# Kernel optimization log

Hardware: AMD Instinct MI355X
Metric: run time of the kernel (lower is better)

The kernel has to match this reference:

```python
import jax, jax.numpy as jnp
import numpy as np
import math

DEPTH = 2
RATIOS = (0.5, 0.5)
K_PROP = 2  # Gra_inc(2)


def _prop(x, ei, ew, K=K_PROP):
    # GCN-style sym-normalized diffusion with implicit self-loops; Gra_inc(K)
    N = x.shape[0]
    row, col = ei[0], ei[1]
    deg = jax.ops.segment_sum(ew, row, num_segments=N) + 1.0  # +1 self-loop
    dinv = jax.lax.rsqrt(deg)
    norm = dinv[row] * ew * dinv[col]          # [E]
    self_n = (dinv * dinv)[:, None]            # [N,1]
    h, out = x, x
    for _ in range(K):
        h = jax.ops.segment_sum(norm[:, None] * h[col], row, num_segments=N) + self_n * h
        out = out + h
    return out


def _conv(x, ei, ew, W):
    return _prop(x @ W, ei, ew)


def _pool(x, ei, ew, pw, ratio):
    # PyG TopKPooling: score = tanh(x.pw/||pw||), keep top ceil(ratio*N) nodes,
    # gate features by score, relabel surviving edges (dropped edges -> weight 0).
    N = x.shape[0]
    k = int(math.ceil(ratio * N))
    score = jnp.tanh(x @ pw / jnp.linalg.norm(pw))
    val, perm = jax.lax.top_k(score, k)
    x2 = x[perm] * val[:, None]
    nm = jnp.full((N,), -1, jnp.int32).at[perm].set(jnp.arange(k, dtype=jnp.int32))
    r, c = nm[ei[0]], nm[ei[1]]
    kept = (r >= 0) & (c >= 0)
    ei2 = jnp.stack([jnp.where(kept, r, 0), jnp.where(kept, c, 0)])
    ew2 = jnp.where(kept, ew, 0.0)
    return x2, ei2, ew2, perm


def setup_inputs() -> dict:
    key = jax.random.key(0)
    ks = jax.random.split(key, 10)
    N, E, C_in, C_hid, C_out = 50000, 800000, 128, 128, 64
    def w(k, i, o):
        return jax.random.normal(k, (i, o), jnp.float32) / np.sqrt(i)
    return {
        "x": jax.random.normal(ks[0], (N, C_in), jnp.float32),
        "edge_index": jax.random.randint(ks[1], (2, E), 0, N, dtype=jnp.int32),
        "Wd0": w(ks[2], C_in, C_hid),
        "Wd1": w(ks[3], C_hid, C_hid),
        "Wd2": w(ks[4], C_hid, C_hid),
        "pw0": jax.random.normal(ks[5], (C_hid,), jnp.float32) / np.sqrt(C_hid),
        "pw1": jax.random.normal(ks[6], (C_hid,), jnp.float32) / np.sqrt(C_hid),
        "Wu0": w(ks[7], C_hid, C_hid),
        "Wu1": w(ks[8], C_hid, C_hid),
        "Wu2": w(ks[9], 2 * C_hid, C_out),
    }


def reference(x, edge_index, Wd0, Wd1, Wd2, pw0, pw1, Wu0, Wu1, Wu2):
    ei = edge_index
    ew = jnp.ones((ei.shape[1],), x.dtype)
    x = jax.nn.relu(_conv(x, ei, ew, Wd0))
    org = x
    xs, eis, ews, perms = [x], [ei], [ew], []
    for i, (pw, Wd) in enumerate(zip((pw0, pw1), (Wd1, Wd2))):
        x, ei, ew, perm = _pool(x, ei, ew, pw, RATIOS[i])
        x = jax.nn.relu(_conv(x, ei, ew, Wd))
        if i < DEPTH - 1:
            xs.append(x); eis.append(ei); ews.append(ew)
        perms.append(perm)
    for i, Wu in enumerate((Wu0, Wu1)):
        j = DEPTH - 1 - i
        res, ei, ew, perm = xs[j], eis[j], ews[j], perms[j]
        up = jnp.zeros_like(res).at[perm].set(x)
        x = res + up  # sum_res skip fusion
        x = _conv(x, ei, ew, Wu)
        if i < DEPTH - 1:
            x = jax.nn.relu(x)
    x = jnp.concatenate([x, org], axis=1)
    return _conv(x, ei, ew, Wu2)
```

## Files before the change

### kernel.cpp

```cpp
#include <hip/hip_runtime.h>
#include <hip/hip_bf16.h>
#include <stdint.h>

#define DEV __device__ __forceinline__

static constexpr int C_HID = 128;

DEV float4 f4_fma(float a, float4 w, float4 acc) {
  acc.x = fmaf(a, w.x, acc.x); acc.y = fmaf(a, w.y, acc.y);
  acc.z = fmaf(a, w.z, acc.z); acc.w = fmaf(a, w.w, acc.w);
  return acc;
}

__global__ void scorekeys_kernel(const float* __restrict__ x, const float* __restrict__ pw,
                                 float* __restrict__ score, unsigned long long* __restrict__ keys,
                                 int N) {
  int row = blockIdx.x * 4 + (threadIdx.x >> 6);
  int lane = threadIdx.x & 63;
  if (row >= N) return;
  float p0 = pw[lane], p1 = pw[lane + 64];
  float pn = p0 * p0 + p1 * p1;
  const float* xr = x + (size_t)row * C_HID;
  float s = xr[lane] * p0 + xr[lane + 64] * p1;
#pragma unroll
  for (int o = 32; o > 0; o >>= 1) {
    s += __shfl_xor(s, o, 64);
    pn += __shfl_xor(pn, o, 64);
  }
  if (lane == 0) {
    float sc = tanhf(s / sqrtf(pn));
    score[row] = sc;
    unsigned u = __float_as_uint(sc);
    u ^= (u >> 31) ? 0xFFFFFFFFu : 0x80000000u;
    keys[row] = (((unsigned long long)(~u)) << 16) | (unsigned)row;
  }
}

__global__ void select_init_kernel(unsigned long long* prefix, int* rem, int k, int* hist3) {
  int i = blockIdx.x * 256 + threadIdx.x;
  if (i == 0) { *prefix = 0ull; *rem = k; }
  for (int j = i; j < 3 * 65536; j += gridDim.x * 256) hist3[j] = 0;
}

__global__ void select_hist_kernel(const unsigned long long* __restrict__ keys, int N,
                                   const unsigned long long* __restrict__ prefix,
                                   int shift, unsigned long long M, int* __restrict__ hist) {
  int i = blockIdx.x * 256 + threadIdx.x;
  if (i >= N) return;
  unsigned long long P = *prefix;
  unsigned long long key = keys[i];
  if (((key ^ P) & M) == 0)
    atomicAdd(&hist[(int)((key >> shift) & 0xFFFF)], 1);
}

__global__ void select_find_kernel(const int* __restrict__ hist,
                                   unsigned long long* __restrict__ prefix,
                                   int* __restrict__ rem, int shift, int* __restrict__ ctr) {
  int t = threadIdx.x;
  int base = t * 64;
  int s = 0;
#pragma unroll
  for (int j = 0; j < 64; ++j) s += hist[base + j];
  int lane = t & 63, w = t >> 6;
  int v = s;
  for (int o = 1; o < 64; o <<= 1) { int u = __shfl_up(v, o, 64); if (lane >= o) v += u; }
  __shared__ int ws[16];
  if (lane == 63) ws[w] = v;
  __syncthreads();
  if (t < 16) {
    int u = ws[t];
    for (int o = 1; o < 16; o <<= 1) { int uu = __shfl_up(u, o, 64); if (t >= o) u += uu; }
    ws[t] = u;
  }
  __syncthreads();
  int incl = v + (w > 0 ? ws[w - 1] : 0);
  int excl = incl - s;
  int R = *rem;
  if (excl < R && incl >= R) {
    int c = excl, b = base;
    for (int j = 0; j < 64; ++j) {
      int h = hist[base + j];
      if (c + h >= R) { b = base + j; break; }
      c += h;
    }
    *prefix |= ((unsigned long long)b) << shift;
    *rem = R - c;
    if (shift == 0) *ctr = 0;
  }
}

__global__ void select_enum_kernel(const unsigned long long* __restrict__ keys, int N,
                                   const unsigned long long* __restrict__ Tptr,
                                   int* __restrict__ ctr, int* __restrict__ perm,
                                   int* __restrict__ nm) {
  int i = blockIdx.x * 256 + threadIdx.x;
  if (i >= N) return;
  unsigned long long T = *Tptr;
  if (keys[i] <= T) { int r = atomicAdd(ctr, 1); perm[r] = i; nm[i] = r; }
  else nm[i] = -1;
}

__global__ void pool_gather_kernel(const float* __restrict__ xold, const float* __restrict__ score,
                                   const int* __restrict__ perm, float* __restrict__ xnew, int k) {
  int j = blockIdx.x * 2 + (threadIdx.x >> 7);
  int f = threadIdx.x & 127;
  if (j >= k) return;
  int src = perm[j];
  xnew[(size_t)j * C_HID + f] = xold[(size_t)src * C_HID + f] * score[src];
}

DEV bool map_edge(int a, int b, const int* m0, const int* m1, int& r, int& c) {
  r = a; c = b;
  if (m0) { r = m0[r]; c = m0[c]; if ((r | c) < 0) return false; }
  if (m1) { r = m1[r]; c = m1[c]; if ((r | c) < 0) return false; }
  return true;
}

__global__ void edge_count_kernel(const int* __restrict__ ei, int E, int* __restrict__ cnt) {
  int e = blockIdx.x * 256 + threadIdx.x;
  if (e >= E) return;
  atomicAdd(&cnt[ei[e]], 1);
}

__global__ void edge_fill_kernel(const int* __restrict__ ei, int E,
                                 const int* __restrict__ rowptr, int* __restrict__ fc,
                                 int* __restrict__ colv) {
  int e = blockIdx.x * 256 + threadIdx.x;
  if (e >= E) return;
  int r = ei[e], c = ei[E + e];
  int pos = rowptr[r] + atomicAdd(&fc[r], 1);
  colv[pos] = c;
}

#define CEPT 7
__global__ __launch_bounds__(1024) void edge_count_compact_kernel(
    const int* __restrict__ ei, int E, const int* m0, const int* m1,
    int* __restrict__ cnt, int2* __restrict__ pairs, int* __restrict__ pctr) {
  int tid = threadIdx.x;
  int gbase = blockIdx.x * (1024 * CEPT) + tid;
  int rs[CEPT], cs[CEPT];
  int myn = 0;
#pragma unroll
  for (int i = 0; i < CEPT; ++i) {
    int e = gbase + i * 1024;
    int r, c;
    bool keep = (e < E) && map_edge(ei[e], ei[E + e], m0, m1, r, c);
    rs[i] = keep ? r : -1;
    cs[i] = keep ? c : 0;
    if (keep) { atomicAdd(&cnt[r], 1); ++myn; }
  }
  int lane = tid & 63, w = tid >> 6;
  int v = myn;
  for (int o = 1; o < 64; o <<= 1) { int u = __shfl_up(v, o, 64); if (lane >= o) v += u; }
  __shared__ int ws[16];
  __shared__ int bbase;
  if (lane == 63) ws[w] = v;
  __syncthreads();
  if (tid < 16) {
    int u = ws[tid];
    for (int o = 1; o < 16; o <<= 1) { int uu = __shfl_up(u, o, 64); if (tid >= o) u += uu; }
    ws[tid] = u;
  }
  __syncthreads();
  int excl = v - myn + (w > 0 ? ws[w - 1] : 0);
  if (tid == 1023) bbase = atomicAdd(pctr, excl + myn);
  __syncthreads();
  int pos = bbase + excl;
#pragma unroll
  for (int i = 0; i < CEPT; ++i)
    if (rs[i] >= 0) pairs[pos++] = make_int2(rs[i], cs[i]);
}

__global__ void edge_fill_compact_kernel(const int2* __restrict__ pairs, const int* __restrict__ pctr,
                                         const int* __restrict__ rowptr, int* __restrict__ fc,
                                         int* __restrict__ colv) {
  int i = blockIdx.x * 256 + threadIdx.x;
  if (i >= *pctr) return;
  int2 pr = pairs[i];
  int pos = rowptr[pr.x] + atomicAdd(&fc[pr.x], 1);
  colv[pos] = pr.y;
}

__global__ void scan_partial_kernel(const int* __restrict__ cnt, int n, int* __restrict__ bsum) {
  int i = blockIdx.x * 256 + threadIdx.x;
  int v = (i < n) ? cnt[i] : 0;
#pragma unroll
  for (int o = 32; o > 0; o >>= 1) v += __shfl_down(v, o, 64);
  __shared__ int ws[4];
  if ((threadIdx.x & 63) == 0) ws[threadIdx.x >> 6] = v;
  __syncthreads();
  if (threadIdx.x == 0) bsum[blockIdx.x] = ws[0] + ws[1] + ws[2] + ws[3];
}

__global__ void scan_blocksums_kernel(int* __restrict__ bsum, int nb) {
  int t = threadIdx.x;
  int v = (t < nb) ? bsum[t] : 0;
  int lane = t & 63, w = t >> 6;
  for (int o = 1; o < 64; o <<= 1) { int u = __shfl_up(v, o, 64); if (lane >= o) v += u; }
  __shared__ int ws[16];
  if (lane == 63) ws[w] = v;
  __syncthreads();
  if (t < 16) {
    int u = ws[t];
    for (int o = 1; o < 16; o <<= 1) { int uu = __shfl_up(u, o, 64); if (t >= o) u += uu; }
    ws[t] = u;
  }
  __syncthreads();
  if (t < nb) bsum[t] = v + (w > 0 ? ws[w - 1] : 0);
}

__global__ void scan_scatter_kernel(const int* __restrict__ cnt, int n,
                                    const int* __restrict__ bsum,
                                    int* __restrict__ rowptr, float* __restrict__ dinv,
                                    int* __restrict__ fc) {
  int i = blockIdx.x * 256 + threadIdx.x;
  int v = (i < n) ? cnt[i] : 0;
  int lane = threadIdx.x & 63, w = threadIdx.x >> 6;
  int s = v;
  for (int o = 1; o < 64; o <<= 1) { int u = __shfl_up(s, o, 64); if (lane >= o) s += u; }
  __shared__ int ws[4];
  __shared__ int wo[4];
  if (lane == 63) ws[w] = s;
  __syncthreads();
  if (threadIdx.x == 0) { int c = 0; for (int j = 0; j < 4; ++j) { wo[j] = c; c += ws[j]; } }
  __syncthreads();
  int excl = s - v + wo[w] + (blockIdx.x > 0 ? bsum[blockIdx.x - 1] : 0);
  if (i < n) {
    rowptr[i] = excl;
    dinv[i] = rsqrtf((float)v + 1.0f);
    fc[i] = 0;
    if (i == n - 1) rowptr[n] = excl + v;
  }
}

template <int FIRST, int RELU>
__global__ void spmm_kernel(const int* __restrict__ rowptr, const int* __restrict__ colv,
                            const float* __restrict__ dinv,
                            const float* __restrict__ h_in, const float* __restrict__ x0,
                            float* __restrict__ out, int M, int C) {
  int lanes = C >> 2;
  int rpb = 256 / lanes;
  int r = blockIdx.x * rpb + (int)threadIdx.x / lanes;
  int lane = (int)threadIdx.x % lanes;
  if (r >= M) return;
  float d = dinv[r];
  const float4* hin4 = (const float4*)h_in;
  size_t base = (size_t)r * lanes + lane;
  float4 self = hin4[base];
  float sn = d * d;
  float4 v = make_float4(sn * self.x, sn * self.y, sn * self.z, sn * self.w);
  int e0 = rowptr[r], e1 = rowptr[r + 1];
  int e = e0;
  for (; e + 8 <= e1; e += 8) {
    int cc[8];
#pragma unroll
    for (int i = 0; i < 8; ++i) cc[i] = colv[e + i];
    float4 hh[8];
#pragma unroll
    for (int i = 0; i < 8; ++i) hh[i] = hin4[(size_t)cc[i] * lanes + lane];
    float ww[8];
#pragma unroll
    for (int i = 0; i < 8; ++i) ww[i] = d * dinv[cc[i]];
#pragma unroll
    for (int i = 0; i < 8; ++i) v = f4_fma(ww[i], hh[i], v);
  }
  for (; e + 4 <= e1; e += 4) {
    int c0 = colv[e], c1 = colv[e + 1], c2 = colv[e + 2], c3 = colv[e + 3];
    float4 h0 = hin4[(size_t)c0 * lanes + lane];
    float4 h1 = hin4[(size_t)c1 * lanes + lane];
    float4 h2 = hin4[(size_t)c2 * lanes + lane];
    float4 h3 = hin4[(size_t)c3 * lanes + lane];
    float w0 = d * dinv[c0], w1 = d * dinv[c1], w2 = d * dinv[c2], w3 = d * dinv[c3];
    v = f4_fma(w0, h0, v); v = f4_fma(w1, h1, v);
    v = f4_fma(w2, h2, v); v = f4_fma(w3, h3, v);
  }
  for (; e < e1; ++e) {
    int c = colv[e];
    float w = d * dinv[c];
    float4 h = hin4[(size_t)c * lanes + lane];
    v = f4_fma(w, h, v);
  }
  if (FIRST) {
    ((float4*)out)[base] = v;
  } else {
    float4 a = ((const float4*)x0)[base];
    a.x += self.x + v.x; a.y += self.y + v.y; a.z += self.z + v.z; a.w += self.w + v.w;
    if (RELU) { a.x = fmaxf(a.x, 0.f); a.y = fmaxf(a.y, 0.f); a.z = fmaxf(a.z, 0.f); a.w = fmaxf(a.w, 0.f); }
    ((float4*)out)[base] = a;
  }
}

template <int NC, int KT, int SKIP, int ADDIN>
__global__ __launch_bounds__(256) void gemm_kernel(const float* __restrict__ A1, int K1,
                                                   const float* __restrict__ W,
                                                   float* __restrict__ Cd, int M,
                                                   const float* __restrict__ up,
                                                   const int* __restrict__ nm,
                                                   const float* __restrict__ addv) {
  constexpr int KTILE = 32;
  constexpr int AP = KTILE + 4;
  constexpr int CG = NC / 4;
  constexpr int RG = 256 / CG;
  constexpr int RPT = 64 / RG;
  __shared__ float Wl[KTILE * NC];
  __shared__ float Al[64 * AP];
  int tid = threadIdx.x;
  int r0 = blockIdx.x * 64;
  int cg = tid % CG, rg = tid / CG;
  float4 acc[RPT];
#pragma unroll
  for (int m = 0; m < RPT; ++m) acc[m] = make_float4(0.f, 0.f, 0.f, 0.f);

  for (int k0 = 0; k0 < KT; k0 += KTILE) {
    const float4* Wg = (const float4*)(W + (size_t)k0 * NC);
    for (int idx = tid; idx < KTILE * NC / 4; idx += 256)
      ((float4*)Wl)[idx] = Wg[idx];
#pragma unroll
    for (int s = 0; s < (64 * KTILE / 4) / 256; ++s) {
      int f4i = tid + s * 256;
      int row = f4i >> 3;
      int kk = (f4i & 7) << 2;
      int gr = r0 + row, gk = k0 + kk;
      float4 v = make_float4(0.f, 0.f, 0.f, 0.f);
      if (gr < M) {
        v = *(const float4*)(A1 + (size_t)gr * K1 + gk);
        if (SKIP) {
          int j = nm[gr];
          if (j >= 0) {
            float4 u = *(const float4*)(up + (size_t)j * K1 + gk);
            v.x += u.x; v.y += u.y; v.z += u.z; v.w += u.w;
          }
        }
      }
      *(float4*)&Al[row * AP + kk] = v;
    }
    __syncthreads();
#pragma unroll
    for (int kk0 = 0; kk0 < KTILE; kk0 += 4) {
      float4 a4[RPT];
#pragma unroll
      for (int m = 0; m < RPT; ++m)
        a4[m] = *(const float4*)&Al[(rg * RPT + m) * AP + kk0];
#pragma unroll
      for (int j = 0; j < 4; ++j) {
        float4 w = *(const float4*)&Wl[(kk0 + j) * NC + cg * 4];
#pragma unroll
        for (int m = 0; m < RPT; ++m) {
          float a = (j == 0) ? a4[m].x : (j == 1) ? a4[m].y : (j == 2) ? a4[m].z : a4[m].w;
          acc[m] = f4_fma(a, w, acc[m]);
        }
      }
    }
    __syncthreads();
  }
#pragma unroll
  for (int m = 0; m < RPT; ++m) {
    int gr = r0 + rg * RPT + m;
    if (gr < M) {
      float4 o = acc[m];
      if (ADDIN) {
        float4 u = *(const float4*)(addv + (size_t)gr * NC + cg * 4);
        o.x += u.x; o.y += u.y; o.z += u.z; o.w += u.w;
      }
      *(float4*)(Cd + (size_t)gr * NC + cg * 4) = o;
    }
  }
}

extern "C" void kernel_launch(void* const* d_in, const int* in_sizes, int n_in,
                              void* d_out, int out_size, void* d_ws, size_t ws_size,
                              hipStream_t stream) {
  const float* x   = (const float*)d_in[0];
  const int*   ei  = (const int*)d_in[1];
  const float* Wd0 = (const float*)d_in[2];
  const float* Wd1 = (const float*)d_in[3];
  const float* Wd2 = (const float*)d_in[4];
  const float* pw0 = (const float*)d_in[5];
  const float* pw1 = (const float*)d_in[6];
  const float* Wu0 = (const float*)d_in[7];
  const float* Wu1 = (const float*)d_in[8];
  const float* Wu2 = (const float*)d_in[9];
  float* out = (float*)d_out;

  const int C = C_HID;
  int N0 = in_sizes[0] / C;
  int E  = in_sizes[1] / 2;
  int k1 = (N0 + 1) / 2;
  int k2 = (k1 + 1) / 2;

  char* p = (char*)d_ws;
  auto alloc = [&](size_t bytes) { char* q = p; p += (bytes + 255) & ~(size_t)255; return q; };
  float* org   = (float*)alloc((size_t)N0 * C * 4);
  float* b0    = (float*)alloc((size_t)N0 * C * 4);
  float* b1    = (float*)alloc((size_t)N0 * C * 4);
  float* b2    = (float*)alloc((size_t)N0 * C * 4);
  float* x1res = (float*)alloc((size_t)k1 * C * 4);
  float* score = (float*)alloc((size_t)N0 * 4);
  unsigned long long* keys = (unsigned long long*)alloc((size_t)N0 * 8);
  int* perm0 = (int*)alloc((size_t)k1 * 4);
  int* perm1 = (int*)alloc((size_t)k2 * 4);
  int* map0  = (int*)alloc((size_t)N0 * 4);
  int* map1  = (int*)alloc((size_t)k1 * 4);
  int* cnt   = (int*)alloc((size_t)N0 * 4);
  int* fc    = (int*)alloc((size_t)N0 * 4);
  int* rp0   = (int*)alloc((size_t)(N0 + 1) * 4);
  int* rp1   = (int*)alloc((size_t)(k1 + 1) * 4);
  int* rp2   = (int*)alloc((size_t)(k2 + 1) * 4);
  float* dinv0 = (float*)alloc((size_t)N0 * 4);
  float* dinv1 = (float*)alloc((size_t)k1 * 4);
  float* dinv2 = (float*)alloc((size_t)k2 * 4);
  int* col0 = (int*)alloc((size_t)E * 4);
  int* col1 = (int*)alloc((size_t)E * 4);
  int* col2 = (int*)alloc((size_t)E * 4);
  int2* pairs = (int2*)alloc((size_t)E * 8);
  int* hist3 = (int*)alloc((size_t)3 * 65536 * 4);
  int* bsum = (int*)alloc(1024 * 4);
  float* Wcat1 = (float*)alloc((size_t)128 * 64 * 4);
  unsigned long long* selT = (unsigned long long*)alloc(64);
  int* selRem = (int*)alloc(64);
  int* selCtr = (int*)alloc(64);
  int* pctr = (int*)alloc(64);

  dim3 b256(256);
  int egrid = (E + 255) / 256;
  int cgrid = (E + 1024 * CEPT - 1) / (1024 * CEPT);
  int g0_128 = (N0 + 7) / 8;
  int g1_128 = (k1 + 7) / 8;
  int g2_128 = (k2 + 7) / 8;
  int g0_64  = (N0 + 15) / 16;

  auto scan_csr = [&](int n, int* rowptr, float* dinv) {
    int g = (n + 255) / 256;
    scan_partial_kernel<<<g, b256, 0, stream>>>(cnt, n, bsum);
    scan_blocksums_kernel<<<1, 1024, 0, stream>>>(bsum, g);
    scan_scatter_kernel<<<g, b256, 0, stream>>>(cnt, n, bsum, rowptr, dinv, fc);
  };

  auto topk_select = [&](int N, int k, int* perm, int* nm) {
    int g = (N + 255) / 256;
    select_init_kernel<<<192, b256, 0, stream>>>(selT, selRem, k, hist3);
    int pass = 0;
    for (int shift = 32; shift >= 0; shift -= 16, ++pass) {
      unsigned long long M = (shift == 32) ? 0ull : (~0ull << (shift + 16));
      select_hist_kernel<<<g, b256, 0, stream>>>(keys, N, selT, shift, M, hist3 + pass * 65536);
      select_find_kernel<<<1, 1024, 0, stream>>>(hist3 + pass * 65536, selT, selRem, shift, selCtr);
    }
    select_enum_kernel<<<g, b256, 0, stream>>>(keys, N, selT, selCtr, perm, nm);
  };

  gemm_kernel<64, 128, 0, 0><<<2, b256, 0, stream>>>(Wu1, 128, Wu2, Wcat1, 128, nullptr, nullptr, nullptr);

  hipMemsetAsync(cnt, 0, (size_t)N0 * 4, stream);
  edge_count_kernel<<<egrid, b256, 0, stream>>>(ei, E, cnt);
  scan_csr(N0, rp0, dinv0);
  edge_fill_kernel<<<egrid, b256, 0, stream>>>(ei, E, rp0, fc, col0);

  gemm_kernel<128, 128, 0, 0><<<(N0 + 63) / 64, b256, 0, stream>>>(x, 128, Wd0, b0, N0, nullptr, nullptr, nullptr);
  spmm_kernel<1, 0><<<g0_128, b256, 0, stream>>>(rp0, col0, dinv0, b0, nullptr, b1, N0, 128);
  spmm_kernel<0, 1><<<g0_128, b256, 0, stream>>>(rp0, col0, dinv0, b1, b0, org, N0, 128);

  scorekeys_kernel<<<(N0 + 3) / 4, b256, 0, stream>>>(org, pw0, score, keys, N0);
  topk_select(N0, k1, perm0, map0);
  pool_gather_kernel<<<(k1 + 1) / 2, b256, 0, stream>>>(org, score, perm0, b0, k1);

  hipMemsetAsync(cnt, 0, (size_t)k1 * 4, stream);
  hipMemsetAsync(pctr, 0, 4, stream);
  edge_count_compact_kernel<<<cgrid, 1024, 0, stream>>>(ei, E, map0, nullptr, cnt, pairs, pctr);
  scan_csr(k1, rp1, dinv1);
  edge_fill_compact_kernel<<<egrid, b256, 0, stream>>>(pairs, pctr, rp1, fc, col1);

  gemm_kernel<128, 128, 0, 0><<<(k1 + 63) / 64, b256, 0, stream>>>(b0, 128, Wd1, b1, k1, nullptr, nullptr, nullptr);
  spmm_kernel<1, 0><<<g1_128, b256, 0, stream>>>(rp1, col1, dinv1, b1, nullptr, b2, k1, 128);
  spmm_kernel<0, 1><<<g1_128, b256, 0, stream>>>(rp1, col1, dinv1, b2, b1, x1res, k1, 128);

  scorekeys_kernel<<<(k1 + 3) / 4, b256, 0, stream>>>(x1res, pw1, score, keys, k1);
  topk_select(k1, k2, perm1, map1);
  pool_gather_kernel<<<(k2 + 1) / 2, b256, 0, stream>>>(x1res, score, perm1, b0, k2);

  hipMemsetAsync(cnt, 0, (size_t)k2 * 4, stream);
  hipMemsetAsync(pctr, 0, 4, stream);
  edge_count_compact_kernel<<<cgrid, 1024, 0, stream>>>(ei, E, map0, map1, cnt, pairs, pctr);
  scan_csr(k2, rp2, dinv2);
  edge_fill_compact_kernel<<<egrid, b256, 0, stream>>>(pairs, pctr, rp2, fc, col2);

  gemm_kernel<128, 128, 0, 0><<<(k2 + 63) / 64, b256, 0, stream>>>(b0, 128, Wd2, b1, k2, nullptr, nullptr, nullptr);
  spmm_kernel<1, 0><<<g2_128, b256, 0, stream>>>(rp2, col2, dinv2, b1, nullptr, b2, k2, 128);
  spmm_kernel<0, 1><<<g2_128, b256, 0, stream>>>(rp2, col2, dinv2, b2, b1, b0, k2, 128);

  gemm_kernel<128, 128, 1, 0><<<(k1 + 63) / 64, b256, 0, stream>>>(x1res, 128, Wu0, b1, k1, b0, map1, nullptr);
  spmm_kernel<1, 0><<<g1_128, b256, 0, stream>>>(rp1, col1, dinv1, b1, nullptr, b2, k1, 128);
  spmm_kernel<0, 1><<<g1_128, b256, 0, stream>>>(rp1, col1, dinv1, b2, b1, b0, k1, 128);

  gemm_kernel<64, 128, 1, 0><<<(N0 + 63) / 64, b256, 0, stream>>>(org, 128, Wcat1, b2, N0, b0, map0, nullptr);
  spmm_kernel<1, 0><<<g0_64, b256, 0, stream>>>(rp0, col0, dinv0, b2, nullptr, b1, N0, 64);
  spmm_kernel<0, 0><<<g0_64, b256, 0, stream>>>(rp0, col0, dinv0, b1, b2, b2, N0, 64);
  gemm_kernel<64, 128, 0, 1><<<(N0 + 63) / 64, b256, 0, stream>>>(org, 128, Wu2 + (size_t)128 * 64, b0, N0, nullptr, nullptr, b2);
  spmm_kernel<1, 0><<<g0_64, b256, 0, stream>>>(rp0, col0, dinv0, b0, nullptr, b1, N0, 64);
  spmm_kernel<0, 0><<<g0_64, b256, 0, stream>>>(rp0, col0, dinv0, b1, b0, out, N0, 64);
}
```

Before: 837.5 us.

## Use bf16 gathered features in up-path SpMM and fuse top-k first histogram

Measured after the change: 914.6 us. +9.2%, slower.

```diff
diff --git a/kernel.cpp b/kernel.cpp
--- a/kernel.cpp
+++ b/kernel.cpp
@@ -12,9 +12,21 @@
   return acc;
 }
 
+DEV unsigned bfpack2(float a, float b) {
+  unsigned ua = __float_as_uint(a), ub = __float_as_uint(b);
+  ua += 0x7FFF + ((ua >> 16) & 1);
+  ub += 0x7FFF + ((ub >> 16) & 1);
+  return (ua >> 16) | (ub & 0xFFFF0000u);
+}
+DEV uint2 bfpack4(float4 v) { return make_uint2(bfpack2(v.x, v.y), bfpack2(v.z, v.w)); }
+DEV float4 bfunpack4(uint2 u) {
+  return make_float4(__uint_as_float(u.x << 16), __uint_as_float(u.x & 0xFFFF0000u),
+                     __uint_as_float(u.y << 16), __uint_as_float(u.y & 0xFFFF0000u));
+}
+
 __global__ void scorekeys_kernel(const float* __restrict__ x, const float* __restrict__ pw,
                                  float* __restrict__ score, unsigned long long* __restrict__ keys,
-                                 int N) {
+                                 int* __restrict__ hist1, int N) {
   int row = blockIdx.x * 4 + (threadIdx.x >> 6);
   int lane = threadIdx.x & 63;
   if (row >= N) return;
@@ -32,14 +44,10 @@
     score[row] = sc;
     unsigned u = __float_as_uint(sc);
     u ^= (u >> 31) ? 0xFFFFFFFFu : 0x80000000u;
-    keys[row] = (((unsigned long long)(~u)) << 16) | (unsigned)row;
-  }
-}
-
-__global__ void select_init_kernel(unsigned long long* prefix, int* rem, int k, int* hist3) {
-  int i = blockIdx.x * 256 + threadIdx.x;
-  if (i == 0) { *prefix = 0ull; *rem = k; }
-  for (int j = i; j < 3 * 65536; j += gridDim.x * 256) hist3[j] = 0;
+    unsigned long long key = (((unsigned long long)(~u)) << 16) | (unsigned)row;
+    keys[row] = key;
+    atomicAdd(&hist1[(int)((key >> 32) & 0xFFFF)], 1);
+  }
 }
 
 __global__ void select_hist_kernel(const unsigned long long* __restrict__ keys, int N,
@@ -55,7 +63,8 @@
 
 __global__ void select_find_kernel(const int* __restrict__ hist,
                                    unsigned long long* __restrict__ prefix,
-                                   int* __restrict__ rem, int shift, int* __restrict__ ctr) {
+                                   int* __restrict__ rem, int shift, int* __restrict__ ctr,
+                                   int k) {
   int t = threadIdx.x;
   int base = t * 64;
   int s = 0;
@@ -75,7 +84,7 @@
   __syncthreads();
   int incl = v + (w > 0 ? ws[w - 1] : 0);
   int excl = incl - s;
-  int R = *rem;
+  int R = (shift == 32) ? k : *rem;
   if (excl < R && incl >= R) {
     int c = excl, b = base;
     for (int j = 0; j < 64; ++j) {
@@ -83,7 +92,8 @@
       if (c + h >= R) { b = base + j; break; }
       c += h;
     }
-    *prefix |= ((unsigned long long)b) << shift;
+    if (shift == 32) *prefix = ((unsigned long long)b) << shift;
+    else             *prefix |= ((unsigned long long)b) << shift;
     *rem = R - c;
     if (shift == 0) *ctr = 0;
   }
@@ -264,16 +274,6 @@
 #pragma unroll
     for (int i = 0; i < 8; ++i) v = f4_fma(ww[i], hh[i], v);
   }
-  for (; e + 4 <= e1; e += 4) {
-    int c0 = colv[e], c1 = colv[e + 1], c2 = colv[e + 2], c3 = colv[e + 3];
-    float4 h0 = hin4[(size_t)c0 * lanes + lane];
-    float4 h1 = hin4[(size_t)c1 * lanes + lane];
-    float4 h2 = hin4[(size_t)c2 * lanes + lane];
-    float4 h3 = hin4[(size_t)c3 * lanes + lane];
-    float w0 = d * dinv[c0], w1 = d * dinv[c1], w2 = d * dinv[c2], w3 = d * dinv[c3];
-    v = f4_fma(w0, h0, v); v = f4_fma(w1, h1, v);
-    v = f4_fma(w2, h2, v); v = f4_fma(w3, h3, v);
-  }
   for (; e < e1; ++e) {
     int c = colv[e];
     float w = d * dinv[c];
@@ -290,13 +290,60 @@
   }
 }
 
-template <int NC, int KT, int SKIP, int ADDIN>
+template <int FIRST, int RELU>
+__global__ void spmm_bf16_kernel(const int* __restrict__ rowptr, const int* __restrict__ colv,
+                                 const float* __restrict__ dinv,
+                                 const ushort* __restrict__ hb, const float* __restrict__ x0,
+                                 void* __restrict__ outp, int M, int C) {
+  int lanes = C >> 2;
+  int rpb = 256 / lanes;
+  int r = blockIdx.x * rpb + (int)threadIdx.x / lanes;
+  int lane = (int)threadIdx.x % lanes;
+  if (r >= M) return;
+  float d = dinv[r];
+  const uint2* hb2 = (const uint2*)hb;
+  size_t base = (size_t)r * lanes + lane;
+  float4 self = bfunpack4(hb2[base]);
+  float sn = d * d;
+  float4 v = make_float4(sn * self.x, sn * self.y, sn * self.z, sn * self.w);
+  int e0 = rowptr[r], e1 = rowptr[r + 1];
+  int e = e0;
+  for (; e + 8 <= e1; e += 8) {
+    int cc[8];
+#pragma unroll
+    for (int i = 0; i < 8; ++i) cc[i] = colv[e + i];
+    uint2 hh[8];
+#pragma unroll
+    for (int i = 0; i < 8; ++i) hh[i] = hb2[(size_t)cc[i] * lanes + lane];
+    float ww[8];
+#pragma unroll
+    for (int i = 0; i < 8; ++i) ww[i] = d * dinv[cc[i]];
+#pragma unroll
+    for (int i = 0; i < 8; ++i) v = f4_fma(ww[i], bfunpack4(hh[i]), v);
+  }
+  for (; e < e1; ++e) {
+    int c = colv[e];
+    float w = d * dinv[c];
+    v = f4_fma(w, bfunpack4(hb2[(size_t)c * lanes + lane]), v);
+  }
+  if (FIRST) {
+    ((uint2*)outp)[base] = bfpack4(v);
+  } else {
+    float4 a = ((const float4*)x0)[base];
+    a.x += self.x + v.x; a.y += self.y + v.y; a.z += self.z + v.z; a.w += self.w + v.w;
+    if (RELU) { a.x = fmaxf(a.x, 0.f); a.y = fmaxf(a.y, 0.f); a.z = fmaxf(a.z, 0.f); a.w = fmaxf(a.w, 0.f); }
+    ((float4*)outp)[base] = a;
+  }
+}
+
+template <int NC, int KT, int SKIP, int ADDIN, int MIRROR>
 __global__ __launch_bounds__(256) void gemm_kernel(const float* __restrict__ A1, int K1,
                                                    const float* __restrict__ W,
                                                    float* __restrict__ Cd, int M,
                                                    const float* __restrict__ up,
                                                    const int* __restrict__ nm,
-                                                   const float* __restrict__ addv) {
+                                                   const float* __restrict__ addv,
+                                                   ushort* __restrict__ bh) {
   constexpr int KTILE = 32;
   constexpr int AP = KTILE + 4;
   constexpr int CG = NC / 4;
@@ -363,6 +410,7 @@
         o.x += u.x; o.y += u.y; o.z += u.z; o.w += u.w;
       }
       *(float4*)(Cd + (size_t)gr * NC + cg * 4) = o;
+      if (MIRROR) ((uint2*)bh)[(size_t)gr * CG + cg] = bfpack4(o);
     }
   }
 }
@@ -395,6 +443,8 @@
   float* b1    = (float*)alloc((size_t)N0 * C * 4);
   float* b2    = (float*)alloc((size_t)N0 * C * 4);
   float* x1res = (float*)alloc((size_t)k1 * C * 4);
+  ushort* bh   = (ushort*)alloc((size_t)N0 * C * 2);
+  ushort* h1h  = (ushort*)alloc((size_t)N0 * C * 2);
   float* score = (float*)alloc((size_t)N0 * 4);
   unsigned long long* keys = (unsigned long long*)alloc((size_t)N0 * 8);
   int* perm0 = (int*)alloc((size_t)k1 * 4);
@@ -413,7 +463,7 @@
   int* col1 = (int*)alloc((size_t)E * 4);
   int* col2 = (int*)alloc((size_t)E * 4);
   int2* pairs = (int2*)alloc((size_t)E * 8);
-  int* hist3 = (int*)alloc((size_t)3 * 65536 * 4);
+  int* hist6 = (int*)alloc((size_t)6 * 65536 * 4);
   int* bsum = (int*)alloc(1024 * 4);
   float* Wcat1 = (float*)alloc((size_t)128 * 64 * 4);
   unsigned long long* selT = (unsigned long long*)alloc(64);
@@ -436,31 +486,31 @@
     scan_scatter_kernel<<<g, b256, 0, stream>>>(cnt, n, bsum, rowptr, dinv, fc);
   };
 
-  auto topk_select = [&](int N, int k, int* perm, int* nm) {
+  auto topk_select = [&](int N, int k, int* perm, int* nm, int* histb) {
     int g = (N + 255) / 256;
-    select_init_kernel<<<192, b256, 0, stream>>>(selT, selRem, k, hist3);
-    int pass = 0;
-    for (int shift = 32; shift >= 0; shift -= 16, ++pass) {
-      unsigned long long M = (shift == 32) ? 0ull : (~0ull << (shift + 16));
-      select_hist_kernel<<<g, b256, 0, stream>>>(keys, N, selT, shift, M, hist3 + pass * 65536);
-      select_find_kernel<<<1, 1024, 0, stream>>>(hist3 + pass * 65536, selT, selRem, shift, selCtr);
-    }
+    select_find_kernel<<<1, 1024, 0, stream>>>(histb, selT, selRem, 32, selCtr, k);
+    select_hist_kernel<<<g, b256, 0, stream>>>(keys, N, selT, 16, ~0ull << 32, histb + 65536);
+    select_find_kernel<<<1, 1024, 0, stream>>>(histb + 65536, selT, selRem, 16, selCtr, k);
+    select_hist_kernel<<<g, b256, 0, stream>>>(keys, N, selT, 0, ~0ull << 16, histb + 2 * 65536);
+    select_find_kernel<<<1, 1024, 0, stream>>>(histb + 2 * 65536, selT, selRem, 0, selCtr, k);
     select_enum_kernel<<<g, b256, 0, stream>>>(keys, N, selT, selCtr, perm, nm);
   };
 
-  gemm_kernel<64, 128, 0, 0><<<2, b256, 0, stream>>>(Wu1, 128, Wu2, Wcat1, 128, nullptr, nullptr, nullptr);
+  hipMemsetAsync(hist6, 0, (size_t)6 * 65536 * 4, stream);
+
+  gemm_kernel<64, 128, 0, 0, 0><<<2, b256, 0, stream>>>(Wu1, 128, Wu2, Wcat1, 128, nullptr, nullptr, nullptr, nullptr);
 
   hipMemsetAsync(cnt, 0, (size_t)N0 * 4, stream);
   edge_count_kernel<<<egrid, b256, 0, stream>>>(ei, E, cnt);
   scan_csr(N0, rp0, dinv0);
   edge_fill_kernel<<<egrid, b256, 0, stream>>>(ei, E, rp0, fc, col0);
 
-  gemm_kernel<128, 128, 0, 0><<<(N0 + 63) / 64, b256, 0, stream>>>(x, 128, Wd0, b0, N0, nullptr, nullptr, nullptr);
+  gemm_kernel<128, 128, 0, 0, 0><<<(N0 + 63) / 64, b256, 0, stream>>>(x, 128, Wd0, b0, N0, nullptr, nullptr, nullptr, nullptr);
   spmm_kernel<1, 0><<<g0_128, b256, 0, stream>>>(rp0, col0, dinv0, b0, nullptr, b1, N0, 128);
   spmm_kernel<0, 1><<<g0_128, b256, 0, stream>>>(rp0, col0, dinv0, b1, b0, org, N0, 128);
 
-  scorekeys_kernel<<<(N0 + 3) / 4, b256, 0, stream>>>(org, pw0, score, keys, N0);
-  topk_select(N0, k1, perm0, map0);
+  scorekeys_kernel<<<(N0 + 3) / 4, b256, 0, stream>>>(org, pw0, score, keys, hist6, N0);
+  topk_select(N0, k1, perm0, map0, hist6);
   pool_gather_kernel<<<(k1 + 1) / 2, b256, 0, stream>>>(org, score, perm0, b0, k1);
 
   hipMemsetAsync(cnt, 0, (size_t)k1 * 4, stream);
@@ -469,12 +519,12 @@
   scan_csr(k1, rp1, dinv1);
   edge_fill_compact_kernel<<<egrid, b256, 0, stream>>>(pairs, pctr, rp1, fc, col1);
 
-  gemm_kernel<128, 128, 0, 0><<<(k1 + 63) / 64, b256, 0, stream>>>(b0, 128, Wd1, b1, k1, nullptr, nullptr, nullptr);
+  gemm_kernel<128, 128, 0, 0, 0><<<(k1 + 63) / 64, b256, 0, stream>>>(b0, 128, Wd1, b1, k1, nullptr, nullptr, nullptr, nullptr);
   spmm_kernel<1, 0><<<g1_128, b256, 0, stream>>>(rp1, col1, dinv1, b1, nullptr, b2, k1, 128);
   spmm_kernel<0, 1><<<g1_128, b256, 0, stream>>>(rp1, col1, dinv1, b2, b1, x1res, k1, 128);
 
-  scorekeys_kernel<<<(k1 + 3) / 4, b256, 0, stream>>>(x1res, pw1, score, keys, k1);
-  topk_select(k1, k2, perm1, map1);
+  scorekeys_kernel<<<(k1 + 3) / 4, b256, 0, stream>>>(x1res, pw1, score, keys, hist6 + 3 * 65536, k1);
+  topk_select(k1, k2, perm1, map1, hist6 + 3 * 65536);
   pool_gather_kernel<<<(k2 + 1) / 2, b256, 0, stream>>>(x1res, score, perm1, b0, k2);
 
   hipMemsetAsync(cnt, 0, (size_t)k2 * 4, stream);
@@ -483,18 +533,18 @@
   scan_csr(k2, rp2, dinv2);
   edge_fill_compact_kernel<<<egrid, b256, 0, stream>>>(pairs, pctr, rp2, fc, col2);
 
-  gemm_kernel<128, 128, 0, 0><<<(k2 + 63) / 64, b256, 0, stream>>>(b0, 128, Wd2, b1, k2, nullptr, nullptr, nullptr);
-  spmm_kernel<1, 0><<<g2_128, b256, 0, stream>>>(rp2, col2, dinv2, b1, nullptr, b2, k2, 128);
-  spmm_kernel<0, 1><<<g2_128, b256, 0, stream>>>(rp2, col2, dinv2, b2, b1, b0, k2, 128);
-
-  gemm_kernel<128, 128, 1, 0><<<(k1 + 63) / 64, b256, 0, stream>>>(x1res, 128, Wu0, b1, k1, b0, map1, nullptr);
-  spmm_kernel<1, 0><<<g1_128, b256, 0, stream>>>(rp1, col1, dinv1, b1, nullptr, b2, k1, 128);
-  spmm_kernel<0, 1><<<g1_128, b256, 0, stream>>>(rp1, col1, dinv1, b2, b1, b0, k1, 128);
-
-  gemm_kernel<64, 128, 1, 0><<<(N0 + 63) / 64, b256, 0, stream>>>(org, 128, Wcat1, b2, N0, b0, map0, nullptr);
-  spmm_kernel<1, 0><<<g0_64, b256, 0, stream>>>(rp0, col0, dinv0, b2, nullptr, b1, N0, 64);
-  spmm_kernel<0, 0><<<g0_64, b256, 0, stream>>>(rp0, col0, dinv0, b1, b2, b2, N0, 64);
-  gemm_kernel<64, 128, 0, 1><<<(N0 + 63) / 64, b256, 0, stream>>>(org, 128, Wu2 + (size_t)128 * 64, b0, N0, nullptr, nullptr, b2);
-  spmm_kernel<1, 0><<<g0_64, b256, 0, stream>>>(rp0, col0, dinv0, b0, nullptr, b1, N0, 64);
-  spmm_kernel<0, 0><<<g0_64, b256, 0, stream>>>(rp0, col0, dinv0, b1, b0, out, N0, 64);
-}
+  gemm_kernel<128, 128, 0, 0, 1><<<(k2 + 63) / 64, b256, 0, stream>>>(b0, 128, Wd2, b1, k2, nullptr, nullptr, nullptr, bh);
+  spmm_bf16_kernel<1, 0><<<g2_128, b256, 0, stream>>>(rp2, col2, dinv2, bh, nullptr, h1h, k2, 128);
+  spmm_bf16_kernel<0, 1><<<g2_128, b256, 0, stream>>>(rp2, col2, dinv2, h1h, b1, b0, k2, 128);
+
+  gemm_kernel<128, 128, 1, 0, 1><<<(k1 + 63) / 64, b256, 0, stream>>>(x1res, 128, Wu0, b1, k1, b0, map1, nullptr, bh);
+  spmm_bf16_kernel<1, 0><<<g1_128, b256, 0, stream>>>(rp1, col1, dinv1, bh, nullptr, h1h, k1, 128);
+  spmm_bf16_kernel<0, 1><<<g1_128, b256, 0, stream>>>(rp1, col1, dinv1, h1h, b1, b0, k1, 128);
+
+  gemm_kernel<64, 128, 1, 0, 1><<<(N0 + 63) / 64, b256, 0, stream>>>(org, 128, Wcat1, b2, N0, b0, map0, nullptr, bh);
+  spmm_bf16_kernel<1, 0><<<g0_64, b256, 0, stream>>>(rp0, col0, dinv0, bh, nullptr, h1h, N0, 64);
+  spmm_bf16_kernel<0, 0><<<g0_64, b256, 0, stream>>>(rp0, col0, dinv0, h1h, b2, b2, N0, 64);
+  gemm_kernel<64, 128, 0, 1, 1><<<(N0 + 63) / 64, b256, 0, stream>>>(org, 128, Wu2 + (size_t)128 * 64, b0, N0, nullptr, nullptr, b2, bh);
+  spmm_bf16_kernel<1, 0><<<g0_64, b256, 0, stream>>>(rp0, col0, dinv0, bh, nullptr, h1h, N0, 64);
+  spmm_bf16_kernel<0, 0><<<g0_64, b256, 0, stream>>>(rp0, col0, dinv0, h1h, b0, out, N0, 64);
+}
```
